# Optimization experiments

Measured on AMD Instinct MI355X. Metric: run time of the kernel, lower is better.

Reference implementation:

```python
import jax, jax.numpy as jnp
import numpy as np

NUM_WIRES = 14
N_LAYERS = 2
BATCH = 256
DIM = 2 ** NUM_WIRES


def setup_inputs() -> dict:
    key = jax.random.key(0)
    k1, k2, k3 = jax.random.split(key, 3)
    s = jax.random.normal(k1, (BATCH, DIM), dtype=jnp.float32)
    # StatePrep requires normalized amplitudes
    s = s / jnp.linalg.norm(s, axis=1, keepdims=True)
    params = jax.random.normal(k2, (N_LAYERS, NUM_WIRES, 3), dtype=jnp.float32)
    head_w = jax.random.normal(k3, (1, NUM_WIRES), dtype=jnp.float32) / np.sqrt(NUM_WIRES)
    head_b = jnp.zeros((1,), dtype=jnp.float32)
    return {"state_batch": s, "params": params, "head_w": head_w, "head_b": head_b}


def _ry(t):
    c = jnp.cos(t / 2).astype(jnp.complex64)
    s = jnp.sin(t / 2).astype(jnp.complex64)
    return jnp.stack([jnp.stack([c, -s]), jnp.stack([s, c])])


def _rz(t):
    tc = t.astype(jnp.complex64)
    e_m = jnp.exp(-0.5j * tc)
    e_p = jnp.exp(0.5j * tc)
    z = jnp.zeros((), jnp.complex64)
    return jnp.stack([jnp.stack([e_m, z]), jnp.stack([z, e_p])])


def _rx(t):
    c = jnp.cos(t / 2).astype(jnp.complex64)
    s = (-1j) * jnp.sin(t / 2).astype(jnp.complex64)
    return jnp.stack([jnp.stack([c, s]), jnp.stack([s, c])])


def _apply_1q(psi, U, wire):
    # psi: (B, 2, 2, ..., 2); contract 2x2 gate on axis wire+1 across the batch
    out = jnp.tensordot(U, psi, axes=([1], [wire + 1]))
    return jnp.moveaxis(out, 0, wire + 1)


def _apply_cnot(psi, control, target):
    # flip target axis where control bit == 1
    shape = [1] * psi.ndim
    shape[control + 1] = 2
    mask = (jnp.arange(2) == 1).reshape(shape)
    return jnp.where(mask, jnp.flip(psi, axis=target + 1), psi)


def _circuit(state_c, params):
    psi = state_c.reshape((BATCH,) + (2,) * NUM_WIRES)
    for layer in range(N_LAYERS):
        for w in range(NUM_WIRES):
            psi = _apply_1q(psi, _ry(params[layer, w, 0]), w)
            psi = _apply_1q(psi, _rz(params[layer, w, 1]), w)
            psi = _apply_cnot(psi, w, (w + 1) % NUM_WIRES)
            psi = _apply_1q(psi, _rx(params[layer, w, 2]), w)
    probs = (psi.real ** 2 + psi.imag ** 2).reshape(BATCH, DIM)
    # <Z_w> = sum over basis states of prob * (+1/-1 depending on bit of wire w)
    basis = jnp.arange(DIM)
    shifts = NUM_WIRES - 1 - jnp.arange(NUM_WIRES)  # wire 0 is the MSB axis
    signs = 1.0 - 2.0 * ((basis[None, :] >> shifts[:, None]) & 1).astype(jnp.float32)
    return probs @ signs.T  # (B, NUM_WIRES)


def reference(state_batch, params, head_w, head_b):
    feats = _circuit(state_batch.astype(jnp.complex64), params)  # (B, NUM_WIRES)
    return feats @ head_w[0] + head_b[0]  # (B,)
```

## Files before the change

### kernel.cpp

```cpp
#include <hip/hip_runtime.h>
#include <math.h>

typedef float v2f __attribute__((ext_vector_type(2)));

constexpr int NW = 14;
constexpr int DIM = 1 << NW;
constexpr int BATCH = 256;
constexpr int NT = 512;

__device__ __host__ constexpr int swzc(int i) {
    return i ^ ((i >> 5) & 31) ^ (((i >> 10) & 15) << 1);
}

template<int Q0,int Q1,int Q2,int Q3,int Q4,int Q5,int Q6,int Q7,int Q8>
__device__ __forceinline__ int scat9(int t) {
    return ((t & 1) << Q0) | (((t >> 1) & 1) << Q1) | (((t >> 2) & 1) << Q2) |
           (((t >> 3) & 1) << Q3) | (((t >> 4) & 1) << Q4) | (((t >> 5) & 1) << Q5) |
           (((t >> 6) & 1) << Q6) | (((t >> 7) & 1) << Q7) | (((t >> 8) & 1) << Q8);
}

template<int JW, int JT>
__device__ __forceinline__ void gate_u(v2f (&pr)[16], v2f (&pi)[16],
                                       float cy, float sy, float c1, float s1,
                                       float cx, float sx)
{
    constexpr int BW = 1 << JW, BT = 1 << JT;
    #pragma unroll
    for (int m = 0; m < 4; ++m) {
        int l00 = 0, mm = m;
        #pragma unroll
        for (int j = 0; j < 4; ++j)
            if (j != JW && j != JT) { l00 |= (mm & 1) << j; mm >>= 1; }
        const int iA = l00, iB = l00 | BW, iC = l00 | BT, iD = l00 | BW | BT;

        v2f a00r = pr[iA], a00i = pi[iA];
        v2f a10r = pr[iB], a10i = pi[iB];
        v2f a01r = pr[iC], a01i = pi[iC];
        v2f a11r = pr[iD], a11i = pi[iD];

        v2f v0r = cy*a00r - sy*a10r, v0i = cy*a00i - sy*a10i;
        v2f v1r = sy*a00r + cy*a10r, v1i = sy*a00i + cy*a10i;
        v2f u0r = cy*a01r - sy*a11r, u0i = cy*a01i - sy*a11i;
        v2f u1r = sy*a01r + cy*a11r, u1i = sy*a01i + cy*a11i;

        v2f b00r = c1*v0r + s1*v0i, b00i = c1*v0i - s1*v0r;
        v2f b10r = c1*v1r - s1*v1i, b10i = c1*v1i + s1*v1r;
        v2f b01r = c1*u0r + s1*u0i, b01i = c1*u0i - s1*u0r;
        v2f b11r = c1*u1r - s1*u1i, b11i = c1*u1i + s1*u1r;

        v2f o00r = cx*b00r + sx*b11i, o00i = cx*b00i - sx*b11r;
        v2f o10r = sx*b00i + cx*b11r, o10i = cx*b11i - sx*b00r;
        v2f o01r = cx*b01r + sx*b10i, o01i = cx*b01i - sx*b10r;
        v2f o11r = sx*b01i + cx*b10r, o11i = cx*b10i - sx*b01r;

        pr[iA] = o00r; pi[iA] = o00i;
        pr[iB] = o10r; pi[iB] = o10i;
        pr[iC] = o01r; pi[iC] = o01i;
        pr[iD] = o11r; pi[iD] = o11i;
    }
}

template<int JT>
__device__ __forceinline__ void gate_w(v2f (&pr)[16], v2f (&pi)[16],
                                       float cy, float sy, float c1, float s1,
                                       float cx, float sx)
{
    constexpr int BT = 1 << JT;
    const v2f K1 = {cy, sy};
    const v2f K2 = {-sy, cy};
    const v2f Zs = {s1, -s1};
    #pragma unroll
    for (int m = 0; m < 8; ++m) {
        int l00 = 0, mm = m;
        #pragma unroll
        for (int j = 0; j < 4; ++j)
            if (j != JT) { l00 |= (mm & 1) << j; mm >>= 1; }
        const int iA = l00, iB = l00 | BT;
        v2f Ar = pr[iA], Ai = pi[iA];
        v2f Br = pr[iB], Bi = pi[iB];

        v2f vAr = K1*Ar.xx + K2*Ar.yy;
        v2f vAi = K1*Ai.xx + K2*Ai.yy;
        v2f vBr = K1*Br.xx + K2*Br.yy;
        v2f vBi = K1*Bi.xx + K2*Bi.yy;
        v2f bAr = c1*vAr + Zs*vAi;
        v2f bAi = c1*vAi - Zs*vAr;
        v2f bBr = c1*vBr + Zs*vBi;
        v2f bBi = c1*vBi - Zs*vBr;
        v2f t1  = {bAr.x, bBr.y};
        v2f t1p = {bBr.x, bAr.y};
        v2f t2  = {bAi.x, bBi.y};
        v2f t2p = {bBi.x, bAi.y};
        pr[iA] = cx*t1  + sx*t2.yx;
        pi[iA] = cx*t2  - sx*t1.yx;
        pr[iB] = cx*t1p + sx*t2p.yx;
        pi[iB] = cx*t2p - sx*t1p.yx;
    }
}

template<int J>
__device__ __forceinline__ void swap_l5(v2f (&pr)[16], v2f (&pi)[16]) {
    #pragma unroll
    for (int m = 0; m < 8; ++m) {
        int l0 = 0, mm = m;
        #pragma unroll
        for (int j = 0; j < 4; ++j)
            if (j != J) { l0 |= (mm & 1) << j; mm >>= 1; }
        const int l1 = l0 | (1 << J);
        { float a=pr[l0].x, c=pr[l1].x; asm("s_nop 1\n\tv_permlane32_swap_b32 %0, %1":"+v"(a),"+v"(c)); pr[l0].x=a; pr[l1].x=c; }
        { float a=pr[l0].y, c=pr[l1].y; asm("s_nop 1\n\tv_permlane32_swap_b32 %0, %1":"+v"(a),"+v"(c)); pr[l0].y=a; pr[l1].y=c; }
        { float a=pi[l0].x, c=pi[l1].x; asm("s_nop 1\n\tv_permlane32_swap_b32 %0, %1":"+v"(a),"+v"(c)); pi[l0].x=a; pi[l1].x=c; }
        { float a=pi[l0].y, c=pi[l1].y; asm("s_nop 1\n\tv_permlane32_swap_b32 %0, %1":"+v"(a),"+v"(c)); pi[l0].y=a; pi[l1].y=c; }
    }
}

template<int J>
__device__ __forceinline__ void swap_l4(v2f (&pr)[16], v2f (&pi)[16]) {
    #pragma unroll
    for (int m = 0; m < 8; ++m) {
        int l0 = 0, mm = m;
        #pragma unroll
        for (int j = 0; j < 4; ++j)
            if (j != J) { l0 |= (mm & 1) << j; mm >>= 1; }
        const int l1 = l0 | (1 << J);
        { float a=pr[l0].x, c=pr[l1].x; asm("s_nop 1\n\tv_permlane16_swap_b32 %0, %1":"+v"(a),"+v"(c)); pr[l0].x=a; pr[l1].x=c; }
        { float a=pr[l0].y, c=pr[l1].y; asm("s_nop 1\n\tv_permlane16_swap_b32 %0, %1":"+v"(a),"+v"(c)); pr[l0].y=a; pr[l1].y=c; }
        { float a=pi[l0].x, c=pi[l1].x; asm("s_nop 1\n\tv_permlane16_swap_b32 %0, %1":"+v"(a),"+v"(c)); pi[l0].x=a; pi[l1].x=c; }
        { float a=pi[l0].y, c=pi[l1].y; asm("s_nop 1\n\tv_permlane16_swap_b32 %0, %1":"+v"(a),"+v"(c)); pi[l0].y=a; pi[l1].y=c; }
    }
}

template<int A0,int A1,int A2,int A3,int PP>
__device__ __forceinline__ void lds_load(const float* re, const float* im,
                                         v2f (&pr)[16], v2f (&pi)[16], int sb) {
    #pragma unroll
    for (int l = 0; l < 16; ++l) {
        const int off = ((l & 1) << A0) | (((l >> 1) & 1) << A1) |
                        (((l >> 2) & 1) << A2) | (((l >> 3) & 1) << A3);
        const int s0 = sb ^ swzc(off);
        const int s1 = sb ^ swzc(off | (1 << PP));
        pr[l] = v2f{re[s0], re[s1]};
        pi[l] = v2f{im[s0], im[s1]};
    }
}

template<int A0,int A1,int A2,int A3,int PP>
__device__ __forceinline__ void lds_store(float* re, float* im,
                                          const v2f (&pr)[16], const v2f (&pi)[16], int sb) {
    #pragma unroll
    for (int l = 0; l < 16; ++l) {
        const int off = ((l & 1) << A0) | (((l >> 1) & 1) << A1) |
                        (((l >> 2) & 1) << A2) | (((l >> 3) & 1) << A3);
        const int s0 = sb ^ swzc(off);
        const int s1 = sb ^ swzc(off | (1 << PP));
        re[s0] = pr[l].x; re[s1] = pr[l].y;
        im[s0] = pi[l].x; im[s1] = pi[l].y;
    }
}

__global__ __launch_bounds__(NT, 1) void qsim(const float* __restrict__ state,
                                              const float* __restrict__ params,
                                              const float* __restrict__ head_w,
                                              const float* __restrict__ head_b,
                                              float* __restrict__ out)
{
    __shared__ float re[DIM];
    __shared__ float im[DIM];
    __shared__ float2 csv[NW * 3 * 2];
    __shared__ float partial[NT / 64];

    const int t = threadIdx.x;
    const int b = blockIdx.x;

    v2f pr[16], pi[16];

    const float* __restrict__ sp = state + (size_t)b * DIM;
    const int tb1 = scat9<0,1,2,3,7,8,4,5,6>(t);
    #pragma unroll
    for (int l = 0; l < 16; ++l) {
        const int off = ((l & 1) << 9) | (((l >> 1) & 1) << 10) |
                        (((l >> 2) & 1) << 11) | (((l >> 3) & 1) << 12);
        pr[l] = v2f{sp[tb1 | off], sp[tb1 | off | (1 << 13)]};
        pi[l] = v2f{0.0f, 0.0f};
    }

    if (t < NW * 3 * 2) {
        float sv, cv;
        sincosf(params[t] * 0.5f, &sv, &cv);
        csv[t] = make_float2(cv, sv);
    }
    __syncthreads();

#define GU(JW, JT, G) do {                                              \
        float2 vy = csv[(G)*3+0], vz = csv[(G)*3+1], vx = csv[(G)*3+2]; \
        gate_u<JW, JT>(pr, pi, vy.x, vy.y, vz.x, vz.y, vx.x, vx.y);     \
    } while (0)
#define GW(JT, G) do {                                                  \
        float2 vy = csv[(G)*3+0], vz = csv[(G)*3+1], vx = csv[(G)*3+2]; \
        gate_w<JT>(pr, pi, vy.x, vy.y, vz.x, vz.y, vx.x, vx.y);         \
    } while (0)

    GW(3, 0);
    GU(3, 2, 1);
    GU(2, 1, 2);
    GU(1, 0, 3);
    swap_l5<3>(pr, pi);
    GU(0, 3, 4);
    swap_l4<0>(pr, pi);
    GU(3, 0, 5);
    lds_store<7,10,11,8,13>(re, im, pr, pi, swzc(scat9<0,1,2,3,9,12,4,5,6>(t)));
    __syncthreads();

    lds_load<3,4,5,6,7>(re, im, pr, pi, swzc(scat9<0,8,9,11,1,2,10,12,13>(t)));
    GW(3, 6);
    GU(3, 2, 7);
    GU(2, 1, 8);
    GU(1, 0, 9);
    swap_l5<3>(pr, pi);
    GU(0, 3, 10);
    swap_l4<2>(pr, pi);
    GU(3, 2, 11);
    lds_store<3,4,1,2,7>(re, im, pr, pi, swzc(scat9<0,8,9,11,5,6,10,12,13>(t)));
    __syncthreads();

    lds_load<0,13,12,11,1>(re, im, pr, pi, swzc(scat9<2,5,6,3,9,10,4,7,8>(t)));
    GW(0, 12);
    GU(0, 1, 13);
    GU(1, 2, 14);
    GU(2, 3, 15);
    swap_l5<1>(pr, pi);
    GU(3, 1, 16);
    swap_l4<0>(pr, pi);
    GU(1, 0, 17);
    lds_store<9,10,12,11,1>(re, im, pr, pi, swzc(scat9<2,5,6,3,0,13,4,7,8>(t)));
    __syncthreads();

    lds_load<8,7,6,5,9>(re, im, pr, pi, swzc(scat9<0,1,2,13,3,4,10,11,12>(t)));
    GW(0, 18);
    GU(0, 1, 19);
    GU(1, 2, 20);
    GU(2, 3, 21);
    swap_l5<0>(pr, pi);
    GU(3, 0, 22);
    swap_l4<1>(pr, pi);
    GU(0, 1, 23);
    lds_store<4,3,6,5,9>(re, im, pr, pi, swzc(scat9<0,1,2,13,7,8,10,11,12>(t)));
    __syncthreads();

    lds_load<2,1,0,13,3>(re, im, pr, pi, swzc(scat9<4,5,6,7,8,9,10,11,12>(t)));
    GW(0, 24);
    GU(0, 1, 25);
    GU(1, 2, 26);
    GU(2, 3, 27);

    float hw[NW];
    #pragma unroll
    for (int w = 0; w < NW; ++w) hw[w] = head_w[w];

    float gbase = 0.0f;
    gbase += (t & 1)   ? -hw[9] : hw[9];
    gbase += (t & 2)   ? -hw[8] : hw[8];
    gbase += (t & 4)   ? -hw[7] : hw[7];
    gbase += (t & 8)   ? -hw[6] : hw[6];
    gbase += (t & 16)  ? -hw[5] : hw[5];
    gbase += (t & 32)  ? -hw[4] : hw[4];
    gbase += (t & 64)  ? -hw[3] : hw[3];
    gbase += (t & 128) ? -hw[2] : hw[2];
    gbase += (t & 256) ? -hw[1] : hw[1];

    v2f acc2 = {0.0f, 0.0f};
    #pragma unroll
    for (int l = 0; l < 16; ++l) {
        float g = gbase;
        g += (l & 1) ? -hw[11] : hw[11];
        g += (l & 2) ? -hw[12] : hw[12];
        g += (l & 4) ? -hw[13] : hw[13];
        g += (l & 8) ? -hw[0]  : hw[0];
        v2f gv = {g + hw[10], g - hw[10]};
        acc2 += (pr[l]*pr[l] + pi[l]*pi[l]) * gv;
    }
    float acc = acc2.x + acc2.y;

    #pragma unroll
    for (int off = 32; off > 0; off >>= 1) acc += __shfl_down(acc, off);
    if ((t & 63) == 0) partial[t >> 6] = acc;
    __syncthreads();
    if (t == 0) {
        float tot = 0.0f;
        #pragma unroll
        for (int k = 0; k < NT / 64; ++k) tot += partial[k];
        out[b] = tot + head_b[0];
    }
#undef GU
#undef GW
}

extern "C" void kernel_launch(void* const* d_in, const int* in_sizes, int n_in,
                              void* d_out, int out_size, void* d_ws, size_t ws_size,
                              hipStream_t stream) {
    const float* state  = (const float*)d_in[0];
    const float* params = (const float*)d_in[1];
    const float* head_w = (const float*)d_in[2];
    const float* head_b = (const float*)d_in[3];
    float* outp = (float*)d_out;
    qsim<<<BATCH, NT, 0, stream>>>(state, params, head_w, head_b, outp);
}
```

Before: 37.56 us.

## Double threads per block, halve per-thread amplitudes, interleave complex LDS storage

Measured after the change: 36.74 us. 2.2% less time.

```diff
diff --git a/kernel.cpp b/kernel.cpp
--- a/kernel.cpp
+++ b/kernel.cpp
@@ -6,31 +6,29 @@
 constexpr int NW = 14;
 constexpr int DIM = 1 << NW;
 constexpr int BATCH = 256;
-constexpr int NT = 512;
-
-__device__ __host__ constexpr int swzc(int i) {
-    return i ^ ((i >> 5) & 31) ^ (((i >> 10) & 15) << 1);
-}
-
-template<int Q0,int Q1,int Q2,int Q3,int Q4,int Q5,int Q6,int Q7,int Q8>
-__device__ __forceinline__ int scat9(int t) {
+constexpr int NT = 1024;
+
+__device__ __host__ constexpr int swz2(int i) {
+    return i ^ ((i >> 4) & 15) ^ ((i >> 8) & 15) ^ ((i >> 12) & 3);
+}
+
+template<int Q0,int Q1,int Q2,int Q3,int Q4,int Q5,int Q6,int Q7,int Q8,int Q9>
+__device__ __forceinline__ int scat10(int t) {
     return ((t & 1) << Q0) | (((t >> 1) & 1) << Q1) | (((t >> 2) & 1) << Q2) |
            (((t >> 3) & 1) << Q3) | (((t >> 4) & 1) << Q4) | (((t >> 5) & 1) << Q5) |
-           (((t >> 6) & 1) << Q6) | (((t >> 7) & 1) << Q7) | (((t >> 8) & 1) << Q8);
+           (((t >> 6) & 1) << Q6) | (((t >> 7) & 1) << Q7) | (((t >> 8) & 1) << Q8) |
+           (((t >> 9) & 1) << Q9);
 }
 
 template<int JW, int JT>
-__device__ __forceinline__ void gate_u(v2f (&pr)[16], v2f (&pi)[16],
+__device__ __forceinline__ void gate_u(v2f (&pr)[8], v2f (&pi)[8],
                                        float cy, float sy, float c1, float s1,
                                        float cx, float sx)
 {
-    constexpr int BW = 1 << JW, BT = 1 << JT;
-    #pragma unroll
-    for (int m = 0; m < 4; ++m) {
-        int l00 = 0, mm = m;
-        #pragma unroll
-        for (int j = 0; j < 4; ++j)
-            if (j != JW && j != JT) { l00 |= (mm & 1) << j; mm >>= 1; }
+    constexpr int BW = 1 << JW, BT = 1 << JT, JF = 3 - JW - JT;
+    #pragma unroll
+    for (int m = 0; m < 2; ++m) {
+        const int l00 = m << JF;
         const int iA = l00, iB = l00 | BW, iC = l00 | BT, iD = l00 | BW | BT;
 
         v2f a00r = pr[iA], a00i = pi[iA];
@@ -61,20 +59,18 @@
 }
 
 template<int JT>
-__device__ __forceinline__ void gate_w(v2f (&pr)[16], v2f (&pi)[16],
+__device__ __forceinline__ void gate_w(v2f (&pr)[8], v2f (&pi)[8],
                                        float cy, float sy, float c1, float s1,
                                        float cx, float sx)
 {
     constexpr int BT = 1 << JT;
+    constexpr int jA = (JT == 0) ? 1 : 0, jB = (JT == 2) ? 1 : 2;
     const v2f K1 = {cy, sy};
     const v2f K2 = {-sy, cy};
     const v2f Zs = {s1, -s1};
     #pragma unroll
-    for (int m = 0; m < 8; ++m) {
-        int l00 = 0, mm = m;
-        #pragma unroll
-        for (int j = 0; j < 4; ++j)
-            if (j != JT) { l00 |= (mm & 1) << j; mm >>= 1; }
+    for (int m = 0; m < 4; ++m) {
+        const int l00 = ((m & 1) << jA) | (((m >> 1) & 1) << jB);
         const int iA = l00, iB = l00 | BT;
         v2f Ar = pr[iA], Ai = pi[iA];
         v2f Br = pr[iB], Bi = pi[iB];
@@ -83,10 +79,12 @@
         v2f vAi = K1*Ai.xx + K2*Ai.yy;
         v2f vBr = K1*Br.xx + K2*Br.yy;
         v2f vBi = K1*Bi.xx + K2*Bi.yy;
+
         v2f bAr = c1*vAr + Zs*vAi;
         v2f bAi = c1*vAi - Zs*vAr;
         v2f bBr = c1*vBr + Zs*vBi;
         v2f bBi = c1*vBi - Zs*vBr;
+
         v2f t1  = {bAr.x, bBr.y};
         v2f t1p = {bBr.x, bAr.y};
         v2f t2  = {bAi.x, bBi.y};
@@ -99,13 +97,11 @@
 }
 
 template<int J>
-__device__ __forceinline__ void swap_l5(v2f (&pr)[16], v2f (&pi)[16]) {
-    #pragma unroll
-    for (int m = 0; m < 8; ++m) {
-        int l0 = 0, mm = m;
-        #pragma unroll
-        for (int j = 0; j < 4; ++j)
-            if (j != J) { l0 |= (mm & 1) << j; mm >>= 1; }
+__device__ __forceinline__ void swap_l5(v2f (&pr)[8], v2f (&pi)[8]) {
+    constexpr int jA = (J == 0) ? 1 : 0, jB = (J == 2) ? 1 : 2;
+    #pragma unroll
+    for (int m = 0; m < 4; ++m) {
+        const int l0 = ((m & 1) << jA) | (((m >> 1) & 1) << jB);
         const int l1 = l0 | (1 << J);
         { float a=pr[l0].x, c=pr[l1].x; asm("s_nop 1\n\tv_permlane32_swap_b32 %0, %1":"+v"(a),"+v"(c)); pr[l0].x=a; pr[l1].x=c; }
         { float a=pr[l0].y, c=pr[l1].y; asm("s_nop 1\n\tv_permlane32_swap_b32 %0, %1":"+v"(a),"+v"(c)); pr[l0].y=a; pr[l1].y=c; }
@@ -115,13 +111,11 @@
 }
 
 template<int J>
-__device__ __forceinline__ void swap_l4(v2f (&pr)[16], v2f (&pi)[16]) {
-    #pragma unroll
-    for (int m = 0; m < 8; ++m) {
-        int l0 = 0, mm = m;
-        #pragma unroll
-        for (int j = 0; j < 4; ++j)
-            if (j != J) { l0 |= (mm & 1) << j; mm >>= 1; }
+__device__ __forceinline__ void swap_l4(v2f (&pr)[8], v2f (&pi)[8]) {
+    constexpr int jA = (J == 0) ? 1 : 0, jB = (J == 2) ? 1 : 2;
+    #pragma unroll
+    for (int m = 0; m < 4; ++m) {
+        const int l0 = ((m & 1) << jA) | (((m >> 1) & 1) << jB);
         const int l1 = l0 | (1 << J);
         { float a=pr[l0].x, c=pr[l1].x; asm("s_nop 1\n\tv_permlane16_swap_b32 %0, %1":"+v"(a),"+v"(c)); pr[l0].x=a; pr[l1].x=c; }
         { float a=pr[l0].y, c=pr[l1].y; asm("s_nop 1\n\tv_permlane16_swap_b32 %0, %1":"+v"(a),"+v"(c)); pr[l0].y=a; pr[l1].y=c; }
@@ -130,31 +124,27 @@
     }
 }
 
-template<int A0,int A1,int A2,int A3,int PP>
-__device__ __forceinline__ void lds_load(const float* re, const float* im,
-                                         v2f (&pr)[16], v2f (&pi)[16], int sb) {
-    #pragma unroll
-    for (int l = 0; l < 16; ++l) {
-        const int off = ((l & 1) << A0) | (((l >> 1) & 1) << A1) |
-                        (((l >> 2) & 1) << A2) | (((l >> 3) & 1) << A3);
-        const int s0 = sb ^ swzc(off);
-        const int s1 = sb ^ swzc(off | (1 << PP));
-        pr[l] = v2f{re[s0], re[s1]};
-        pi[l] = v2f{im[s0], im[s1]};
-    }
-}
-
-template<int A0,int A1,int A2,int A3,int PP>
-__device__ __forceinline__ void lds_store(float* re, float* im,
-                                          const v2f (&pr)[16], const v2f (&pi)[16], int sb) {
-    #pragma unroll
-    for (int l = 0; l < 16; ++l) {
-        const int off = ((l & 1) << A0) | (((l >> 1) & 1) << A1) |
-                        (((l >> 2) & 1) << A2) | (((l >> 3) & 1) << A3);
-        const int s0 = sb ^ swzc(off);
-        const int s1 = sb ^ swzc(off | (1 << PP));
-        re[s0] = pr[l].x; re[s1] = pr[l].y;
-        im[s0] = pi[l].x; im[s1] = pi[l].y;
+template<int S0,int S1,int S2,int PP>
+__device__ __forceinline__ void lds_store(float2* cs,
+                                          const v2f (&pr)[8], const v2f (&pi)[8], int sb) {
+    #pragma unroll
+    for (int k = 0; k < 8; ++k) {
+        const int off = ((k & 1) << S0) | (((k >> 1) & 1) << S1) | (((k >> 2) & 1) << S2);
+        cs[sb ^ swz2(off)]             = float2{pr[k].x, pi[k].x};
+        cs[sb ^ swz2(off | (1 << PP))] = float2{pr[k].y, pi[k].y};
+    }
+}
+
+template<int S0,int S1,int S2,int PP>
+__device__ __forceinline__ void lds_load(const float2* cs,
+                                         v2f (&pr)[8], v2f (&pi)[8], int sb) {
+    #pragma unroll
+    for (int k = 0; k < 8; ++k) {
+        const int off = ((k & 1) << S0) | (((k >> 1) & 1) << S1) | (((k >> 2) & 1) << S2);
+        const float2 a0 = cs[sb ^ swz2(off)];
+        const float2 a1 = cs[sb ^ swz2(off | (1 << PP))];
+        pr[k] = v2f{a0.x, a1.x};
+        pi[k] = v2f{a0.y, a1.y};
     }
 }
 
@@ -164,24 +154,22 @@
                                               const float* __restrict__ head_b,
                                               float* __restrict__ out)
 {
-    __shared__ float re[DIM];
-    __shared__ float im[DIM];
+    __shared__ float2 cs[DIM];
     __shared__ float2 csv[NW * 3 * 2];
     __shared__ float partial[NT / 64];
 
     const int t = threadIdx.x;
     const int b = blockIdx.x;
 
-    v2f pr[16], pi[16];
+    v2f pr[8], pi[8];
 
     const float* __restrict__ sp = state + (size_t)b * DIM;
-    const int tb1 = scat9<0,1,2,3,7,8,4,5,6>(t);
-    #pragma unroll
-    for (int l = 0; l < 16; ++l) {
-        const int off = ((l & 1) << 9) | (((l >> 1) & 1) << 10) |
-                        (((l >> 2) & 1) << 11) | (((l >> 3) & 1) << 12);
-        pr[l] = v2f{sp[tb1 | off], sp[tb1 | off | (1 << 13)]};
-        pi[l] = v2f{0.0f, 0.0f};
+    const int tbA = scat10<0,1,2,3,8,9,4,5,6,7>(t);
+    #pragma unroll
+    for (int k = 0; k < 8; ++k) {
+        const int base = tbA | (k << 10);
+        pr[k] = v2f{sp[base], sp[base | (1 << 13)]};
+        pi[k] = v2f{0.0f, 0.0f};
     }
 
     if (t < NW * 3 * 2) {
@@ -200,84 +188,92 @@
         gate_w<JT>(pr, pi, vy.x, vy.y, vz.x, vz.y, vx.x, vx.y);         \
     } while (0)
 
-    GW(3, 0);
-    GU(3, 2, 1);
-    GU(2, 1, 2);
-    GU(1, 0, 3);
-    swap_l5<3>(pr, pi);
-    GU(0, 3, 4);
-    swap_l4<0>(pr, pi);
-    GU(3, 0, 5);
-    lds_store<7,10,11,8,13>(re, im, pr, pi, swzc(scat9<0,1,2,3,9,12,4,5,6>(t)));
-    __syncthreads();
-
-    lds_load<3,4,5,6,7>(re, im, pr, pi, swzc(scat9<0,8,9,11,1,2,10,12,13>(t)));
-    GW(3, 6);
-    GU(3, 2, 7);
-    GU(2, 1, 8);
-    GU(1, 0, 9);
-    swap_l5<3>(pr, pi);
-    GU(0, 3, 10);
-    swap_l4<2>(pr, pi);
-    GU(3, 2, 11);
-    lds_store<3,4,1,2,7>(re, im, pr, pi, swzc(scat9<0,8,9,11,5,6,10,12,13>(t)));
-    __syncthreads();
-
-    lds_load<0,13,12,11,1>(re, im, pr, pi, swzc(scat9<2,5,6,3,9,10,4,7,8>(t)));
-    GW(0, 12);
-    GU(0, 1, 13);
-    GU(1, 2, 14);
-    GU(2, 3, 15);
-    swap_l5<1>(pr, pi);
-    GU(3, 1, 16);
-    swap_l4<0>(pr, pi);
-    GU(1, 0, 17);
-    lds_store<9,10,12,11,1>(re, im, pr, pi, swzc(scat9<2,5,6,3,0,13,4,7,8>(t)));
-    __syncthreads();
-
-    lds_load<8,7,6,5,9>(re, im, pr, pi, swzc(scat9<0,1,2,13,3,4,10,11,12>(t)));
-    GW(0, 18);
-    GU(0, 1, 19);
-    GU(1, 2, 20);
-    GU(2, 3, 21);
-    swap_l5<0>(pr, pi);
-    GU(3, 0, 22);
+    GW(2, 0);
+    GU(2, 1, 1);
+    GU(1, 0, 2);
+    swap_l5<2>(pr, pi);
+    GU(0, 2, 3);
     swap_l4<1>(pr, pi);
-    GU(0, 1, 23);
-    lds_store<4,3,6,5,9>(re, im, pr, pi, swzc(scat9<0,1,2,13,7,8,10,11,12>(t)));
-    __syncthreads();
-
-    lds_load<2,1,0,13,3>(re, im, pr, pi, swzc(scat9<4,5,6,7,8,9,10,11,12>(t)));
-    GW(0, 24);
-    GU(0, 1, 25);
-    GU(1, 2, 26);
-    GU(2, 3, 27);
+    GU(2, 1, 4);
+    lds_store<10,8,9,13>(cs, pr, pi, swz2(scat10<0,1,2,3,11,12,4,5,6,7>(t)));
+    __syncthreads();
+
+    const int sbB = swz2(scat10<0,1,2,9,3,4,10,11,12,13>(t));
+    lds_load<5,6,7,8>(cs, pr, pi, sbB);
+    GW(2, 5);
+    GU(2, 1, 6);
+    GU(1, 0, 7);
+    swap_l5<2>(pr, pi);
+    GU(0, 2, 8);
+    swap_l4<1>(pr, pi);
+    GU(2, 1, 9);
+    lds_store<5,3,4,8>(cs, pr, pi, swz2(scat10<0,1,2,9,6,7,10,11,12,13>(t)));
+    __syncthreads();
+
+    const int sbC = swz2(scat10<4,5,6,7,9,13,8,10,11,12>(t));
+    lds_load<0,1,2,3>(cs, pr, pi, sbC);
+    GW(2, 10);
+    GU(2, 1, 11);
+    GU(1, 0, 12);
+    swap_l5<2>(pr, pi);
+    GU(0, 2, 13);
+    lds_store<0,1,13,3>(cs, pr, pi, swz2(scat10<4,5,6,7,9,2,8,10,11,12>(t)));
+    __syncthreads();
+
+    lds_load<10,11,12,13>(cs, pr, pi, swz2(tbA));
+    GW(2, 14);
+    GU(2, 1, 15);
+    GU(1, 0, 16);
+    swap_l5<2>(pr, pi);
+    GU(0, 2, 17);
+    swap_l4<1>(pr, pi);
+    GU(2, 1, 18);
+    lds_store<10,8,9,13>(cs, pr, pi, swz2(scat10<0,1,2,3,11,12,4,5,6,7>(t)));
+    __syncthreads();
+
+    lds_load<5,6,7,8>(cs, pr, pi, sbB);
+    GW(2, 19);
+    GU(2, 1, 20);
+    GU(1, 0, 21);
+    swap_l5<2>(pr, pi);
+    GU(0, 2, 22);
+    swap_l4<1>(pr, pi);
+    GU(2, 1, 23);
+    lds_store<5,3,4,8>(cs, pr, pi, swz2(scat10<0,1,2,9,6,7,10,11,12,13>(t)));
+    __syncthreads();
+
+    lds_load<0,1,2,3>(cs, pr, pi, sbC);
+    GW(2, 24);
+    GU(2, 1, 25);
+    GU(1, 0, 26);
+    swap_l5<2>(pr, pi);
+    GU(0, 2, 27);
 
     float hw[NW];
     #pragma unroll
     for (int w = 0; w < NW; ++w) hw[w] = head_w[w];
 
     float gbase = 0.0f;
-    gbase += (t & 1)   ? -hw[9] : hw[9];
-    gbase += (t & 2)   ? -hw[8] : hw[8];
-    gbase += (t & 4)   ? -hw[7] : hw[7];
-    gbase += (t & 8)   ? -hw[6] : hw[6];
-    gbase += (t & 16)  ? -hw[5] : hw[5];
-    gbase += (t & 32)  ? -hw[4] : hw[4];
-    gbase += (t & 64)  ? -hw[3] : hw[3];
-    gbase += (t & 128) ? -hw[2] : hw[2];
-    gbase += (t & 256) ? -hw[1] : hw[1];
+    gbase += (t & 1)   ? -hw[9]  : hw[9];
+    gbase += (t & 2)   ? -hw[8]  : hw[8];
+    gbase += (t & 4)   ? -hw[7]  : hw[7];
+    gbase += (t & 8)   ? -hw[6]  : hw[6];
+    gbase += (t & 16)  ? -hw[4]  : hw[4];
+    gbase += (t & 32)  ? -hw[11] : hw[11];
+    gbase += (t & 64)  ? -hw[5]  : hw[5];
+    gbase += (t & 128) ? -hw[3]  : hw[3];
+    gbase += (t & 256) ? -hw[2]  : hw[2];
+    gbase += (t & 512) ? -hw[1]  : hw[1];
 
     v2f acc2 = {0.0f, 0.0f};
     #pragma unroll
-    for (int l = 0; l < 16; ++l) {
+    for (int k = 0; k < 8; ++k) {
         float g = gbase;
-        g += (l & 1) ? -hw[11] : hw[11];
-        g += (l & 2) ? -hw[12] : hw[12];
-        g += (l & 4) ? -hw[13] : hw[13];
-        g += (l & 8) ? -hw[0]  : hw[0];
+        g += (k & 1) ? -hw[13] : hw[13];
+        g += (k & 2) ? -hw[12] : hw[12];
+        g += (k & 4) ? -hw[0]  : hw[0];
         v2f gv = {g + hw[10], g - hw[10]};
-        acc2 += (pr[l]*pr[l] + pi[l]*pi[l]) * gv;
+        acc2 += (pr[k]*pr[k] + pi[k]*pi[k]) * gv;
     }
     float acc = acc2.x + acc2.y;
 
```
